# Kernel optimization log

Hardware: AMD Instinct MI355X
Metric: run time of the kernel (lower is better)

The kernel has to match this reference:

```python
import jax, jax.numpy as jnp
import numpy as np

LEVELS = [(128, 128), (64, 64), (32, 32), (16, 16)]  # (H_l, W_l) per feature level
N_TOTAL = sum(h * w for h, w in LEVELS)  # 21760
B, D, H, P, L = 2, 256, 8, 4, 4
HD = D // H
FFN_DIM = 1024


def setup_inputs() -> dict:
    key = jax.random.key(0)
    ks = jax.random.split(key, 12)
    s = 0.02  # weight init scale
    return {
        'embed': jax.random.normal(ks[0], (B, N_TOTAL, D), jnp.float32),
        'pos': jax.random.normal(ks[1], (B, N_TOTAL, D), jnp.float32),
        'ref_points': jax.random.uniform(ks[2], (B, N_TOTAL, L, 2), jnp.float32),
        'ln1_w': jnp.ones((D,), jnp.float32), 'ln1_b': jnp.zeros((D,), jnp.float32),
        'ln2_w': jnp.ones((D,), jnp.float32), 'ln2_b': jnp.zeros((D,), jnp.float32),
        'Wv': jax.random.normal(ks[3], (D, D), jnp.float32) * s, 'bv': jnp.zeros((D,), jnp.float32),
        'Woff': jax.random.normal(ks[4], (D, H * L * P * 2), jnp.float32) * s, 'boff': jnp.zeros((H * L * P * 2,), jnp.float32),
        'Wattn': jax.random.normal(ks[5], (D, H * L * P), jnp.float32) * s, 'battn': jnp.zeros((H * L * P,), jnp.float32),
        'Wo': jax.random.normal(ks[6], (D, D), jnp.float32) * s, 'bo': jnp.zeros((D,), jnp.float32),
        'W1': jax.random.normal(ks[7], (D, FFN_DIM), jnp.float32) * s, 'b1': jnp.zeros((FFN_DIM,), jnp.float32),
        'W2': jax.random.normal(ks[8], (FFN_DIM, D), jnp.float32) * s, 'b2': jnp.zeros((D,), jnp.float32),
        'dimensions': jnp.array(LEVELS, jnp.int32),
    }


def _layer_norm(x, w, b):
    m = jnp.mean(x, axis=-1, keepdims=True)
    v = jnp.mean(jnp.square(x - m), axis=-1, keepdims=True)
    return (x - m) * jax.lax.rsqrt(v + 1e-5) * w + b


def _msda(q, ref, v, dims, Wv, bv, Woff, boff, Wattn, battn, Wo, bo):
    # q, v: (B, N, D); ref: (B, N, L, 2) normalized (x, y)
    Bq, N, _ = q.shape
    value = (v @ Wv + bv).reshape(Bq, N, H, HD)
    off = (q @ Woff + boff).reshape(Bq, N, H, L, P, 2)
    aw = jax.nn.softmax((q @ Wattn + battn).reshape(Bq, N, H, L * P), axis=-1)
    aw = aw.reshape(Bq, N, H, L, P)
    # offset normalizer is [W_l, H_l]
    norm = jnp.stack([dims[:, 1], dims[:, 0]], axis=-1).astype(q.dtype)  # (L, 2)
    loc = ref[:, :, None, :, None, :] + off / norm[None, None, None, :, None, :]  # (B,N,H,L,P,2)

    out = jnp.zeros((Bq, N, H, HD), q.dtype)
    start = 0
    for l, (Hl, Wl) in enumerate(LEVELS):
        S = Hl * Wl
        vl = value[:, start:start + S].transpose(0, 2, 1, 3)  # (B, H, S, hd)
        start += S
        # grid_sample semantics: align_corners=False, zero padding
        x = loc[:, :, :, l, :, 0] * Wl - 0.5  # (B, N, H, P)
        y = loc[:, :, :, l, :, 1] * Hl - 0.5
        x0 = jnp.floor(x); y0 = jnp.floor(y)
        wx = x - x0; wy = y - y0
        x0i = x0.astype(jnp.int32); y0i = y0.astype(jnp.int32)
        samp = jnp.zeros(x.shape + (HD,), q.dtype)
        for dy, dx, w in ((0, 0, (1 - wx) * (1 - wy)), (0, 1, wx * (1 - wy)),
                          (1, 0, (1 - wx) * wy), (1, 1, wx * wy)):
            xi = x0i + dx; yi = y0i + dy
            valid = (xi >= 0) & (xi < Wl) & (yi >= 0) & (yi < Hl)
            idx = jnp.clip(yi, 0, Hl - 1) * Wl + jnp.clip(xi, 0, Wl - 1)  # (B, N, H, P)
            idx_t = idx.transpose(0, 2, 1, 3).reshape(Bq, H, N * P)
            g = jnp.take_along_axis(vl, idx_t[..., None], axis=2)  # (B, H, N*P, hd)
            g = g.reshape(Bq, H, N, P, HD).transpose(0, 2, 1, 3, 4)  # (B, N, H, P, hd)
            samp = samp + (w * valid)[..., None] * g
        out = out + jnp.sum(samp * aw[:, :, :, l, :, None], axis=3)
    return out.reshape(Bq, N, D) @ Wo + bo


def reference(embed, pos, ref_points, ln1_w, ln1_b, ln2_w, ln2_b, Wv, bv, Woff, boff,
              Wattn, battn, Wo, bo, W1, b1, W2, b2, dimensions):
    v = _layer_norm(embed, ln1_w, ln1_b)
    q = v + pos
    embed = embed + _msda(q, ref_points, v, dimensions, Wv, bv, Woff, boff, Wattn, battn, Wo, bo)
    f = _layer_norm(embed, ln2_w, ln2_b)
    embed = embed + jax.nn.relu(f @ W1 + b1) @ W2 + b2
    return embed
```

## Files before the change

### kernel.cpp

```cpp
#include <hip/hip_runtime.h>
#include <cstdint>
#include <cstddef>

#define N_TOTAL 21760
#define BATCH   2
#define M_TOT   (BATCH * N_TOTAL)
#define DMODEL  256
#define NHEAD   8
#define HDIM    32
#define FFN     1024

typedef __bf16 b16x8 __attribute__((ext_vector_type(8)));
typedef float  f32x4 __attribute__((ext_vector_type(4)));

typedef const __attribute__((address_space(1))) void g_void;
typedef __attribute__((address_space(3))) void lds_void;

__device__ __forceinline__ unsigned short f2b(float f) {
  union { float f; unsigned u; } v; v.f = f;
  unsigned r = v.u + 0x7FFF + ((v.u >> 16) & 1);
  return (unsigned short)(r >> 16);
}
__device__ __forceinline__ float b2f(unsigned short u) {
  union { unsigned u; float f; } v; v.u = (unsigned)u << 16;
  return v.f;
}

__device__ __forceinline__ int xcd_wgid(int bid, int nwg) {
  int q = nwg >> 3, r = nwg & 7;
  int xcd = bid & 7, k = bid >> 3;
  return (xcd < r ? xcd * (q + 1) : r * (q + 1) + (xcd - r) * q) + k;
}

__global__ void wconv_all(const float* __restrict__ Wv, const float* __restrict__ Woff,
                          const float* __restrict__ Wattn, const float* __restrict__ Wo,
                          const float* __restrict__ W1, const float* __restrict__ W2,
                          unsigned short* __restrict__ dstbase) {
  int idx = blockIdx.x * 256 + threadIdx.x;
  const float* src; int K, N, off;
  if (idx < 65536)       { src = Wv;    K = 256;  N = 256;  off = 0;      }
  else if (idx < 131072) { src = Woff;  K = 256;  N = 256;  off = 65536;  idx -= 65536; }
  else if (idx < 163840) { src = Wattn; K = 256;  N = 128;  off = 131072; idx -= 131072; }
  else if (idx < 229376) { src = Wo;    K = 256;  N = 256;  off = 163840; idx -= 163840; }
  else if (idx < 491520) { src = W1;    K = 256;  N = 1024; off = 229376; idx -= 229376; }
  else if (idx < 753664) { src = W2;    K = 1024; N = 256;  off = 491520; idx -= 491520; }
  else return;
  int k = idx / N, n = idx - k * N;
  dstbase[off + (size_t)n * K + k] = f2b(src[idx]);
}

__global__ void ln1_kernel(const float* __restrict__ x, const float* __restrict__ pos,
                           const float* __restrict__ w, const float* __restrict__ b,
                           unsigned short* __restrict__ vb, unsigned short* __restrict__ qb) {
  int t = threadIdx.x;
  int tkn = blockIdx.x * 4 + (t >> 6);
  int lane = t & 63;
  size_t base = (size_t)tkn * DMODEL + lane * 4;
  float4 xv = *(const float4*)&x[base];
  float s1 = xv.x + xv.y + xv.z + xv.w;
  float s2 = xv.x * xv.x + xv.y * xv.y + xv.z * xv.z + xv.w * xv.w;
  #pragma unroll
  for (int off = 32; off; off >>= 1) {
    s1 += __shfl_down(s1, off);
    s2 += __shfl_down(s2, off);
  }
  s1 = __shfl(s1, 0); s2 = __shfl(s2, 0);
  float m   = s1 * (1.0f / DMODEL);
  float var = s2 * (1.0f / DMODEL) - m * m;
  float rs  = rsqrtf(var + 1e-5f);
  float4 wv = *(const float4*)&w[lane * 4];
  float4 bv = *(const float4*)&b[lane * 4];
  float4 pv = *(const float4*)&pos[base];
  float o0 = (xv.x - m) * rs * wv.x + bv.x;
  float o1 = (xv.y - m) * rs * wv.y + bv.y;
  float o2 = (xv.z - m) * rs * wv.z + bv.z;
  float o3 = (xv.w - m) * rs * wv.w + bv.w;
  ushort4 vo = {f2b(o0), f2b(o1), f2b(o2), f2b(o3)};
  ushort4 qo = {f2b(o0 + pv.x), f2b(o1 + pv.y), f2b(o2 + pv.z), f2b(o3 + pv.w)};
  *(ushort4*)&vb[base] = vo;
  *(ushort4*)&qb[base] = qo;
}

__global__ void ln2_kernel(const unsigned short* __restrict__ x, const float* __restrict__ w,
                           const float* __restrict__ b, unsigned short* __restrict__ yb) {
  int t = threadIdx.x;
  int tkn = blockIdx.x * 4 + (t >> 6);
  int lane = t & 63;
  size_t base = (size_t)tkn * DMODEL + lane * 4;
  ushort4 xu = *(const ushort4*)&x[base];
  float x0 = b2f(xu.x), x1 = b2f(xu.y), x2 = b2f(xu.z), x3 = b2f(xu.w);
  float s1 = x0 + x1 + x2 + x3;
  float s2 = x0 * x0 + x1 * x1 + x2 * x2 + x3 * x3;
  #pragma unroll
  for (int off = 32; off; off >>= 1) {
    s1 += __shfl_down(s1, off);
    s2 += __shfl_down(s2, off);
  }
  s1 = __shfl(s1, 0); s2 = __shfl(s2, 0);
  float m   = s1 * (1.0f / DMODEL);
  float var = s2 * (1.0f / DMODEL) - m * m;
  float rs  = rsqrtf(var + 1e-5f);
  float4 wv = *(const float4*)&w[lane * 4];
  float4 bv = *(const float4*)&b[lane * 4];
  ushort4 vo = {f2b((x0 - m) * rs * wv.x + bv.x), f2b((x1 - m) * rs * wv.y + bv.y),
                f2b((x2 - m) * rs * wv.z + bv.z), f2b((x3 - m) * rs * wv.w + bv.w)};
  *(ushort4*)&yb[base] = vo;
}

__device__ __forceinline__ void gemm_core(
    const unsigned short* __restrict__ A, const unsigned short* __restrict__ Bt,
    const float* __restrict__ bias,
    const float* __restrict__ addf, const unsigned short* __restrict__ addb,
    float* __restrict__ Cf, unsigned short* __restrict__ Cb,
    int K, int N, int relu, int row0, int col0,
    unsigned short* As, unsigned short* Bs) {
  int t  = threadIdx.x;
  int w  = t >> 6;
  int l  = t & 63;
  int wm = w >> 1, wn = w & 1;
  int lr = l & 15;
  int kq = l >> 4;

  f32x4 acc[4][4];
  #pragma unroll
  for (int i = 0; i < 4; ++i)
    #pragma unroll
    for (int j = 0; j < 4; ++j) acc[i][j] = (f32x4){0.f, 0.f, 0.f, 0.f};

  int srow = (l >> 3);
  int sseg = (l & 7) * 8;

  for (int k0 = 0; k0 < K; k0 += 64) {
    #pragma unroll
    for (int i = 0; i < 4; ++i) {
      int c = w * 4 + i;
      const unsigned short* ga = A  + (size_t)(row0 + c * 8 + srow) * K + k0 + sseg;
      const unsigned short* gb = Bt + (size_t)(col0 + c * 8 + srow) * K + k0 + sseg;
      __builtin_amdgcn_global_load_lds((g_void*)ga, (lds_void*)(As + c * 512), 16, 0, 0);
      __builtin_amdgcn_global_load_lds((g_void*)gb, (lds_void*)(Bs + c * 512), 16, 0, 0);
    }
    __syncthreads();
    #pragma unroll
    for (int kk = 0; kk < 2; ++kk) {
      b16x8 aF[4], bF[4];
      #pragma unroll
      for (int i = 0; i < 4; ++i)
        aF[i] = *(const b16x8*)&As[(wm * 64 + i * 16 + lr) * 64 + kk * 32 + kq * 8];
      #pragma unroll
      for (int j = 0; j < 4; ++j)
        bF[j] = *(const b16x8*)&Bs[(wn * 64 + j * 16 + lr) * 64 + kk * 32 + kq * 8];
      #pragma unroll
      for (int i = 0; i < 4; ++i)
        #pragma unroll
        for (int j = 0; j < 4; ++j)
          acc[i][j] = __builtin_amdgcn_mfma_f32_16x16x32_bf16(aF[i], bF[j], acc[i][j], 0, 0, 0);
    }
    __syncthreads();
  }

  #pragma unroll
  for (int j = 0; j < 4; ++j) {
    int colg = col0 + wn * 64 + j * 16 + lr;
    float bcol = bias[colg];
    #pragma unroll
    for (int i = 0; i < 4; ++i) {
      int r0g = row0 + wm * 64 + i * 16 + kq * 4;
      #pragma unroll
      for (int r = 0; r < 4; ++r) {
        int rowg = r0g + r;
        float o = acc[i][j][r] + bcol;
        if (relu) o = fmaxf(o, 0.0f);
        if (addf) o += addf[(size_t)rowg * N + colg];
        if (addb) o += b2f(addb[(size_t)rowg * N + colg]);
        if (Cf) Cf[(size_t)rowg * N + colg] = o;
        if (Cb) Cb[(size_t)rowg * N + colg] = f2b(o);
      }
    }
  }
}

__global__ __launch_bounds__(256, 3)
void gemm_bf16(const unsigned short* __restrict__ A,
               const unsigned short* __restrict__ Bt,
               const float* __restrict__ bias,
               const float* __restrict__ addf, const unsigned short* __restrict__ addb,
               float* __restrict__ Cf, unsigned short* __restrict__ Cb,
               int K, int N, int relu, int ncolt) {
  __shared__ unsigned short As[128 * 64];
  __shared__ unsigned short Bs[128 * 64];
  int wgid = xcd_wgid(blockIdx.x, gridDim.x);
  int row0 = (wgid / ncolt) * 128;
  int col0 = (wgid % ncolt) * 128;
  gemm_core(A, Bt, bias, addf, addb, Cf, Cb, K, N, relu, row0, col0, As, Bs);
}

__global__ __launch_bounds__(256, 3)
void gemm_proj(const unsigned short* __restrict__ vb,
               const unsigned short* __restrict__ qb,
               const unsigned short* __restrict__ Wvt,
               const unsigned short* __restrict__ Wofft,
               const unsigned short* __restrict__ Wattnt,
               const float* __restrict__ bv, const float* __restrict__ boff,
               const float* __restrict__ battn,
               unsigned short* __restrict__ valb,
               unsigned short* __restrict__ offb,
               unsigned short* __restrict__ awb) {
  __shared__ unsigned short As[128 * 64];
  __shared__ unsigned short Bs[128 * 64];
  int wgid = xcd_wgid(blockIdx.x, gridDim.x);
  int y = wgid % 5;
  int row0 = (wgid / 5) * 128;
  const unsigned short* A; const unsigned short* Bt; const float* bias;
  unsigned short* C; int col0, N;
  if (y < 2)      { A = vb; Bt = Wvt;    bias = bv;    C = valb; col0 = y * 128;       N = 256; }
  else if (y < 4) { A = qb; Bt = Wofft;  bias = boff;  C = offb; col0 = (y - 2) * 128; N = 256; }
  else            { A = qb; Bt = Wattnt; bias = battn; C = awb;  col0 = 0;             N = 128; }
  gemm_core(A, Bt, bias, nullptr, nullptr, nullptr, C, 256, N, 0, row0, col0, As, Bs);
}

__global__ void msda_kernel(const unsigned short* __restrict__ value,
                            const unsigned short* __restrict__ offb,
                            const unsigned short* __restrict__ awb,
                            const float* __restrict__ ref,
                            unsigned short* __restrict__ outb) {
  __shared__ int2 P[544];
  int bid = blockIdx.x;
  int tkn = (bid & 7) * (M_TOT / 8) + (bid >> 3);
  int t   = threadIdx.x;
  int b   = (tkn >= N_TOTAL) ? 1 : 0;

  if (t < 128) {
    int h = t >> 4, s = t & 15, lev = s >> 2, p = s & 3;
    float lg = b2f(awb[(size_t)tkn * 128 + h * 16 + s]);
    float mx = lg;
    #pragma unroll
    for (int m = 1; m < 16; m <<= 1) mx = fmaxf(mx, __shfl_xor(mx, m, 16));
    float e = __expf(lg - mx);
    float sum = e;
    #pragma unroll
    for (int m = 1; m < 16; m <<= 1) sum += __shfl_xor(sum, m, 16);
    float aw = e / sum;

    const int HL[4] = {128, 64, 32, 16};
    const int ST[4] = {0, 16384, 20480, 21504};
    int Wl = HL[lev];
    float rx = ref[(size_t)tkn * 8 + lev * 2 + 0];
    float ry = ref[(size_t)tkn * 8 + lev * 2 + 1];
    float ox = b2f(offb[(size_t)tkn * 256 + h * 32 + lev * 8 + p * 2 + 0]);
    float oy = b2f(offb[(size_t)tkn * 256 + h * 32 + lev * 8 + p * 2 + 1]);
    float x = rx * (float)Wl + ox - 0.5f;
    float y = ry * (float)Wl + oy - 0.5f;
    float x0f = floorf(x), y0f = floorf(y);
    float wx = x - x0f, wy = y - y0f;
    int x0 = (int)x0f, y0 = (int)y0f;
    float wt[4] = {(1.f - wx) * (1.f - wy), wx * (1.f - wy),
                   (1.f - wx) * wy, wx * wy};
    int base = b * N_TOTAL + ST[lev];
    #pragma unroll
    for (int tp = 0; tp < 4; ++tp) {
      int e4 = s * 4 + tp;
      int idx = h * 68 + (e4 >> 5) * 34 + (e4 & 31);
      int xi = x0 + (tp & 1), yi = y0 + (tp >> 1);
      bool ok = (xi >= 0) & (xi < Wl) & (yi >= 0) & (yi < Wl);
      float wgt = ok ? aw * wt[tp] : 0.f;
      int boff2 = ok ? (((base + yi * Wl + xi) * 256 + h * 32) * 2) : 0;
      P[idx] = (int2){__float_as_int(wgt), boff2};
    }
  }
  __syncthreads();

  int h = t >> 5, g = t & 31, dp = g & 15, half = g >> 4;
  int o = h * 68 + half * 34;
  unsigned doff = dp * 4;
  const char* vbase = (const char*)value;
  float accL = 0.f, accH = 0.f;
  #pragma unroll 8
  for (int j = 0; j < 32; ++j) {
    int2 pr = P[o + j];
    float wgt = __int_as_float(pr.x);
    unsigned v = *(const unsigned*)(vbase + (size_t)((unsigned)pr.y + doff));
    union { unsigned u; float f; } lo, hi;
    lo.u = v << 16;
    hi.u = v & 0xffff0000u;
    accL += wgt * lo.f;
    accH += wgt * hi.f;
  }
  accL += __shfl_xor(accL, 16);
  accH += __shfl_xor(accH, 16);
  if (half == 0) {
    unsigned pk = (unsigned)f2b(accL) | ((unsigned)f2b(accH) << 16);
    *(unsigned*)&outb[(size_t)tkn * 256 + h * 32 + dp * 2] = pk;
  }
}

extern "C" void kernel_launch(void* const* d_in, const int* in_sizes, int n_in,
                              void* d_out, int out_size, void* d_ws, size_t ws_size,
                              hipStream_t stream) {
  const float* embed = (const float*)d_in[0];
  const float* pos   = (const float*)d_in[1];
  const float* refp  = (const float*)d_in[2];
  const float* ln1w  = (const float*)d_in[3];
  const float* ln1b  = (const float*)d_in[4];
  const float* ln2w  = (const float*)d_in[5];
  const float* ln2b  = (const float*)d_in[6];
  const float* Wv    = (const float*)d_in[7];
  const float* bv    = (const float*)d_in[8];
  const float* Woff  = (const float*)d_in[9];
  const float* boff  = (const float*)d_in[10];
  const float* Wattn = (const float*)d_in[11];
  const float* battn = (const float*)d_in[12];
  const float* Wo    = (const float*)d_in[13];
  const float* bo    = (const float*)d_in[14];
  const float* W1    = (const float*)d_in[15];
  const float* b1    = (const float*)d_in[16];
  const float* W2    = (const float*)d_in[17];
  const float* b2    = (const float*)d_in[18];
  float* out = (float*)d_out;
  float* ws  = (float*)d_ws;

  const size_t U = (size_t)M_TOT * DMODEL;
  unsigned short* valb16 = (unsigned short*)ws;
  unsigned short* offb16 = (unsigned short*)(ws + U / 2);
  unsigned short* awb16  = (unsigned short*)(ws + U);
  unsigned short* msdab  = (unsigned short*)(ws + U + U / 4);
  unsigned short* hid16  = (unsigned short*)ws;
  unsigned short* emb2b  = (unsigned short*)(ws + 2 * U);
  unsigned short* vb16   = (unsigned short*)(ws + 3 * U);
  unsigned short* qb16   = (unsigned short*)(ws + 3 * U + U / 2);
  unsigned short* fb16   = (unsigned short*)(ws + 4 * U);
  unsigned short* wbuf   = (unsigned short*)(ws + 4 * U + U / 2);

  unsigned short* Wvt    = wbuf;
  unsigned short* Wofft  = wbuf + 65536;
  unsigned short* Wattnt = wbuf + 131072;
  unsigned short* Wot    = wbuf + 163840;
  unsigned short* W1t    = wbuf + 229376;
  unsigned short* W2t    = wbuf + 491520;

  wconv_all<<<(753664 + 255) / 256, 256, 0, stream>>>(Wv, Woff, Wattn, Wo, W1, W2, wbuf);

  ln1_kernel<<<M_TOT / 4, 256, 0, stream>>>(embed, pos, ln1w, ln1b, vb16, qb16);

  gemm_proj<<<(M_TOT / 128) * 5, 256, 0, stream>>>(
      vb16, qb16, Wvt, Wofft, Wattnt, bv, boff, battn, valb16, offb16, awb16);

  msda_kernel<<<M_TOT, 256, 0, stream>>>(valb16, offb16, awb16, refp, msdab);

  gemm_bf16<<<(M_TOT / 128) * 2, 256, 0, stream>>>(
      msdab, Wot, bo, embed, nullptr, nullptr, emb2b, 256, 256, 0, 2);

  ln2_kernel<<<M_TOT / 4, 256, 0, stream>>>(emb2b, ln2w, ln2b, fb16);

  gemm_bf16<<<(M_TOT / 128) * 8, 256, 0, stream>>>(
      fb16, W1t, b1, nullptr, nullptr, nullptr, hid16, 256, 1024, 1, 8);
  gemm_bf16<<<(M_TOT / 128) * 2, 256, 0, stream>>>(
      hid16, W2t, b2, nullptr, emb2b, out, nullptr, 1024, 256, 0, 2);
}
```

Measured before the change: 304.2 us.

## Fuse output projection with residual add and LayerNorm2; vectorize MSDA pair loads

```diff
diff --git a/kernel.cpp b/kernel.cpp
--- a/kernel.cpp
+++ b/kernel.cpp
@@ -79,32 +79,6 @@
   ushort4 qo = {f2b(o0 + pv.x), f2b(o1 + pv.y), f2b(o2 + pv.z), f2b(o3 + pv.w)};
   *(ushort4*)&vb[base] = vo;
   *(ushort4*)&qb[base] = qo;
-}
-
-__global__ void ln2_kernel(const unsigned short* __restrict__ x, const float* __restrict__ w,
-                           const float* __restrict__ b, unsigned short* __restrict__ yb) {
-  int t = threadIdx.x;
-  int tkn = blockIdx.x * 4 + (t >> 6);
-  int lane = t & 63;
-  size_t base = (size_t)tkn * DMODEL + lane * 4;
-  ushort4 xu = *(const ushort4*)&x[base];
-  float x0 = b2f(xu.x), x1 = b2f(xu.y), x2 = b2f(xu.z), x3 = b2f(xu.w);
-  float s1 = x0 + x1 + x2 + x3;
-  float s2 = x0 * x0 + x1 * x1 + x2 * x2 + x3 * x3;
-  #pragma unroll
-  for (int off = 32; off; off >>= 1) {
-    s1 += __shfl_down(s1, off);
-    s2 += __shfl_down(s2, off);
-  }
-  s1 = __shfl(s1, 0); s2 = __shfl(s2, 0);
-  float m   = s1 * (1.0f / DMODEL);
-  float var = s2 * (1.0f / DMODEL) - m * m;
-  float rs  = rsqrtf(var + 1e-5f);
-  float4 wv = *(const float4*)&w[lane * 4];
-  float4 bv = *(const float4*)&b[lane * 4];
-  ushort4 vo = {f2b((x0 - m) * rs * wv.x + bv.x), f2b((x1 - m) * rs * wv.y + bv.y),
-                f2b((x2 - m) * rs * wv.z + bv.z), f2b((x3 - m) * rs * wv.w + bv.w)};
-  *(ushort4*)&yb[base] = vo;
 }
 
 __device__ __forceinline__ void gemm_core(
@@ -218,12 +192,138 @@
   gemm_core(A, Bt, bias, nullptr, nullptr, nullptr, C, 256, N, 0, row0, col0, As, Bs);
 }
 
+__global__ __launch_bounds__(512, 2)
+void gemm_wo_ln2(const unsigned short* __restrict__ A,
+                 const unsigned short* __restrict__ Bt,
+                 const float* __restrict__ bias,
+                 const float* __restrict__ emb,
+                 const float* __restrict__ lnw, const float* __restrict__ lnb,
+                 unsigned short* __restrict__ emb2b,
+                 unsigned short* __restrict__ fb16) {
+  __shared__ unsigned short As[128 * 64];
+  __shared__ unsigned short Bs[256 * 64];
+  __shared__ float lnS1[128 * 4], lnS2[128 * 4];
+  __shared__ float lnM[128], lnR[128];
+  int t  = threadIdx.x;
+  int w  = t >> 6;
+  int l  = t & 63;
+  int wm = w >> 2, wn = w & 3;
+  int lr = l & 15;
+  int kq = l >> 4;
+  int row0 = xcd_wgid(blockIdx.x, gridDim.x) * 128;
+
+  f32x4 acc[4][4];
+  #pragma unroll
+  for (int i = 0; i < 4; ++i)
+    #pragma unroll
+    for (int j = 0; j < 4; ++j) acc[i][j] = (f32x4){0.f, 0.f, 0.f, 0.f};
+
+  int srow = (l >> 3);
+  int sseg = (l & 7) * 8;
+
+  for (int k0 = 0; k0 < 256; k0 += 64) {
+    #pragma unroll
+    for (int i = 0; i < 2; ++i) {
+      int c = w * 2 + i;
+      const unsigned short* ga = A + (size_t)(row0 + c * 8 + srow) * 256 + k0 + sseg;
+      __builtin_amdgcn_global_load_lds((g_void*)ga, (lds_void*)(As + c * 512), 16, 0, 0);
+    }
+    #pragma unroll
+    for (int i = 0; i < 4; ++i) {
+      int c = w * 4 + i;
+      const unsigned short* gb = Bt + (size_t)(c * 8 + srow) * 256 + k0 + sseg;
+      __builtin_amdgcn_global_load_lds((g_void*)gb, (lds_void*)(Bs + c * 512), 16, 0, 0);
+    }
+    __syncthreads();
+    #pragma unroll
+    for (int kk = 0; kk < 2; ++kk) {
+      b16x8 aF[4], bF[4];
+      #pragma unroll
+      for (int i = 0; i < 4; ++i)
+        aF[i] = *(const b16x8*)&As[(wm * 64 + i * 16 + lr) * 64 + kk * 32 + kq * 8];
+      #pragma unroll
+      for (int j = 0; j < 4; ++j)
+        bF[j] = *(const b16x8*)&Bs[(wn * 64 + j * 16 + lr) * 64 + kk * 32 + kq * 8];
+      #pragma unroll
+      for (int i = 0; i < 4; ++i)
+        #pragma unroll
+        for (int j = 0; j < 4; ++j)
+          acc[i][j] = __builtin_amdgcn_mfma_f32_16x16x32_bf16(aF[i], bF[j], acc[i][j], 0, 0, 0);
+    }
+    __syncthreads();
+  }
+
+  float s1[4][4] = {}, s2[4][4] = {};
+  #pragma unroll
+  for (int j = 0; j < 4; ++j) {
+    int colg = wn * 64 + j * 16 + lr;
+    float bcol = bias[colg];
+    #pragma unroll
+    for (int i = 0; i < 4; ++i) {
+      int rowg = row0 + wm * 64 + i * 16 + kq * 4;
+      #pragma unroll
+      for (int r = 0; r < 4; ++r) {
+        float o = acc[i][j][r] + bcol + emb[(size_t)(rowg + r) * 256 + colg];
+        acc[i][j][r] = o;
+        s1[i][r] += o;
+        s2[i][r] += o * o;
+      }
+    }
+  }
+  #pragma unroll
+  for (int m = 1; m < 16; m <<= 1) {
+    #pragma unroll
+    for (int i = 0; i < 4; ++i)
+      #pragma unroll
+      for (int r = 0; r < 4; ++r) {
+        s1[i][r] += __shfl_xor(s1[i][r], m);
+        s2[i][r] += __shfl_xor(s2[i][r], m);
+      }
+  }
+  if (lr == 0) {
+    #pragma unroll
+    for (int i = 0; i < 4; ++i)
+      #pragma unroll
+      for (int r = 0; r < 4; ++r) {
+        int rl = wm * 64 + i * 16 + kq * 4 + r;
+        lnS1[rl * 4 + wn] = s1[i][r];
+        lnS2[rl * 4 + wn] = s2[i][r];
+      }
+  }
+  __syncthreads();
+  if (t < 128) {
+    float a = lnS1[t * 4] + lnS1[t * 4 + 1] + lnS1[t * 4 + 2] + lnS1[t * 4 + 3];
+    float b = lnS2[t * 4] + lnS2[t * 4 + 1] + lnS2[t * 4 + 2] + lnS2[t * 4 + 3];
+    float m = a * (1.0f / 256.0f);
+    float var = b * (1.0f / 256.0f) - m * m;
+    lnM[t] = m;
+    lnR[t] = rsqrtf(var + 1e-5f);
+  }
+  __syncthreads();
+  #pragma unroll
+  for (int i = 0; i < 4; ++i) {
+    #pragma unroll
+    for (int r = 0; r < 4; ++r) {
+      int rl = wm * 64 + i * 16 + kq * 4 + r;
+      float m = lnM[rl], rs = lnR[rl];
+      int rowg = row0 + rl;
+      #pragma unroll
+      for (int j = 0; j < 4; ++j) {
+        int colg = wn * 64 + j * 16 + lr;
+        float o = acc[i][j][r];
+        emb2b[(size_t)rowg * 256 + colg] = f2b(o);
+        fb16[(size_t)rowg * 256 + colg] = f2b((o - m) * rs * lnw[colg] + lnb[colg]);
+      }
+    }
+  }
+}
+
 __global__ void msda_kernel(const unsigned short* __restrict__ value,
                             const unsigned short* __restrict__ offb,
                             const unsigned short* __restrict__ awb,
                             const float* __restrict__ ref,
                             unsigned short* __restrict__ outb) {
-  __shared__ int2 P[544];
+  __shared__ int2 P[544] __attribute__((aligned(16)));
   int bid = blockIdx.x;
   int tkn = (bid & 7) * (M_TOT / 8) + (bid >> 3);
   int t   = threadIdx.x;
@@ -274,16 +374,18 @@
   unsigned doff = dp * 4;
   const char* vbase = (const char*)value;
   float accL = 0.f, accH = 0.f;
-  #pragma unroll 8
-  for (int j = 0; j < 32; ++j) {
-    int2 pr = P[o + j];
-    float wgt = __int_as_float(pr.x);
-    unsigned v = *(const unsigned*)(vbase + (size_t)((unsigned)pr.y + doff));
-    union { unsigned u; float f; } lo, hi;
-    lo.u = v << 16;
-    hi.u = v & 0xffff0000u;
-    accL += wgt * lo.f;
-    accH += wgt * hi.f;
+  #pragma unroll 4
+  for (int j2 = 0; j2 < 16; ++j2) {
+    int4 pr2 = *(const int4*)&P[o + j2 * 2];
+    float wgt0 = __int_as_float(pr2.x);
+    float wgt1 = __int_as_float(pr2.z);
+    unsigned v0 = *(const unsigned*)(vbase + (size_t)((unsigned)pr2.y + doff));
+    unsigned v1 = *(const unsigned*)(vbase + (size_t)((unsigned)pr2.w + doff));
+    union { unsigned u; float f; } l0, h0, l1, h1;
+    l0.u = v0 << 16; h0.u = v0 & 0xffff0000u;
+    l1.u = v1 << 16; h1.u = v1 & 0xffff0000u;
+    accL += wgt0 * l0.f + wgt1 * l1.f;
+    accH += wgt0 * h0.f + wgt1 * h1.f;
   }
   accL += __shfl_xor(accL, 16);
   accH += __shfl_xor(accH, 16);
@@ -346,10 +448,8 @@
 
   msda_kernel<<<M_TOT, 256, 0, stream>>>(valb16, offb16, awb16, refp, msdab);
 
-  gemm_bf16<<<(M_TOT / 128) * 2, 256, 0, stream>>>(
-      msdab, Wot, bo, embed, nullptr, nullptr, emb2b, 256, 256, 0, 2);
-
-  ln2_kernel<<<M_TOT / 4, 256, 0, stream>>>(emb2b, ln2w, ln2b, fb16);
+  gemm_wo_ln2<<<M_TOT / 128, 512, 0, stream>>>(
+      msdab, Wot, bo, embed, ln2w, ln2b, emb2b, fb16);
 
   gemm_bf16<<<(M_TOT / 128) * 8, 256, 0, stream>>>(
       fb16, W1t, b1, nullptr, nullptr, nullptr, hid16, 256, 1024, 1, 8);
```

After: 301.3 us. No clear change (-1.0%).
